# Performance work log

Measured on AMD Instinct MI355X. Metric: run time of the kernel, lower is better.

Reference implementation:

```python
import jax, jax.numpy as jnp
import numpy as np
import math

D_MODEL = 1024
N_HEAD = 16
D_HEAD = D_MODEL // N_HEAD


def setup_inputs() -> dict:
    key = jax.random.key(0)
    k0, k1, k2, k3, k4 = jax.random.split(key, 5)
    B, N = 4, 2048
    inp = jax.random.normal(k0, (B, N, D_MODEL), dtype=jnp.float32)
    # causal mask: True = keep (masked_fill on ~mask)
    mask = jnp.tril(jnp.ones((N, N), dtype=bool))
    # qkv_proj Linear(d_model, 3*d_model); output Linear(d_model, d_model)
    s_in = 1.0 / math.sqrt(D_MODEL)
    W_qkv = jax.random.uniform(k1, (D_MODEL, 3 * D_MODEL), jnp.float32, -s_in, s_in)
    b_qkv = jax.random.uniform(k2, (3 * D_MODEL,), jnp.float32, -s_in, s_in)
    W_out = jax.random.uniform(k3, (D_MODEL, D_MODEL), jnp.float32, -s_in, s_in)
    b_out = jax.random.uniform(k4, (D_MODEL,), jnp.float32, -s_in, s_in)
    return {"input": inp, "W_qkv": W_qkv, "b_qkv": b_qkv,
            "W_out": W_out, "b_out": b_out, "mask": mask}


def reference(input, W_qkv, b_qkv, W_out, b_out, mask):
    B, N, d = input.shape
    qkv = input @ W_qkv + b_qkv                       # [B,N,3d]  (dropout=eval no-op)
    q, k, v = jnp.split(qkv, 3, axis=-1)
    # [B,N,H,Dh] -> [B,H,N,Dh]
    q = q.reshape(B, N, N_HEAD, D_HEAD).transpose(0, 2, 1, 3)
    k = k.reshape(B, N, N_HEAD, D_HEAD).transpose(0, 2, 1, 3)
    v = v.reshape(B, N, N_HEAD, D_HEAD).transpose(0, 2, 1, 3)
    scale = 1.0 / math.sqrt(D_HEAD)
    scores = jnp.einsum('bhqd,bhkd->bhqk', q, k) * scale   # [B,H,N,N]
    scores = jnp.where(mask, scores, -jnp.inf)
    attn = jax.nn.softmax(scores, axis=-1)
    out = jnp.einsum('bhqk,bhkd->bhqd', attn, v)           # [B,H,N,Dh]
    out = out.transpose(0, 2, 1, 3).reshape(B, N, d)       # concat heads
    return out @ W_out + b_out
```

## Files before the change

kernel.cpp:

```cpp
#include <hip/hip_runtime.h>
#include <hip/hip_bf16.h>

typedef unsigned short u16;
typedef unsigned u32;
typedef __attribute__((ext_vector_type(4))) unsigned short u16x4;
typedef __attribute__((ext_vector_type(8))) unsigned short u16x8;
typedef __attribute__((ext_vector_type(4))) unsigned u32x4;
typedef __attribute__((ext_vector_type(8))) __bf16 bf16x8;
typedef __attribute__((ext_vector_type(4))) float f32x4;

typedef __attribute__((address_space(1))) void as1v;
typedef __attribute__((address_space(3))) void as3v;

#define MFMA16(a, b, c) __builtin_amdgcn_mfma_f32_16x16x32_bf16(a, b, c, 0, 0, 0)

__device__ __forceinline__ u16 f2bf(float f) {
    unsigned u = __builtin_bit_cast(unsigned, f);
    u += 0x7fffu + ((u >> 16) & 1u);
    return (u16)(u >> 16);
}

__device__ __forceinline__ u32 pkbf(float lo, float hi) {
    u32 r;
    asm("v_cvt_pk_bf16_f32 %0, %1, %2" : "=v"(r) : "v"(lo), "v"(hi));
    return r;
}

__device__ __forceinline__ void gload16(const void* g, void* l) {
    __builtin_amdgcn_global_load_lds((as1v*)g, (as3v*)l, 16, 0, 0);
}

__global__ void convert_f32_bf16(const float* __restrict__ in, u16* __restrict__ out, int n4) {
    int i = blockIdx.x * blockDim.x + threadIdx.x;
    if (i < n4) {
        float4 v = *(const float4*)&in[(size_t)i * 4];
        u16x4 o;
        o.x = f2bf(v.x); o.y = f2bf(v.y); o.z = f2bf(v.z); o.w = f2bf(v.w);
        *(u16x4*)&out[(size_t)i * 4] = o;
    }
}

__global__ void transpose_convert(const float* __restrict__ in, u16* __restrict__ out, int R, int C) {
    __shared__ float tl[64][65];
    const int rb = blockIdx.x, cb = blockIdx.y;
    const int tid = threadIdx.x;
    for (int it = 0; it < 4; ++it) {
        int lin = (tid + it * 256) * 4;
        int r = lin >> 6, c = lin & 63;
        float4 v = *(const float4*)&in[(size_t)(rb * 64 + r) * C + cb * 64 + c];
        tl[r][c + 0] = v.x; tl[r][c + 1] = v.y; tl[r][c + 2] = v.z; tl[r][c + 3] = v.w;
    }
    __syncthreads();
    for (int it = 0; it < 4; ++it) {
        int lin = (tid + it * 256) * 4;
        int oc = lin >> 6, orr = lin & 63;
        u16x4 o;
        o.x = f2bf(tl[orr + 0][oc]);
        o.y = f2bf(tl[orr + 1][oc]);
        o.z = f2bf(tl[orr + 2][oc]);
        o.w = f2bf(tl[orr + 3][oc]);
        *(u16x4*)&out[(size_t)(cb * 64 + oc) * R + rb * 64 + orr] = o;
    }
}

__global__ void transpose_v(const u16* __restrict__ vbuf, u16* __restrict__ vtb) {
    __shared__ u16 tl[64][65];
    const int nb = blockIdx.x, bh = blockIdx.y;
    const int tid = threadIdx.x;
    for (int it = 0; it < 2; ++it) {
        int lin = (tid + it * 256) * 8;
        int nl = lin >> 6, dh = lin & 63;
        u16x8 v = *(const u16x8*)&vbuf[((size_t)bh * 2048 + nb * 64 + nl) * 64 + dh];
#pragma unroll
        for (int j = 0; j < 8; ++j) tl[dh + j][nl] = v[j];
    }
    __syncthreads();
    for (int it = 0; it < 2; ++it) {
        int lin = (tid + it * 256) * 8;
        int dh = lin >> 6, nl = lin & 63;
        u16x8 o;
#pragma unroll
        for (int j = 0; j < 8; ++j) o[j] = tl[dh][nl + j];
        *(u16x8*)&vtb[((size_t)bh * 64 + dh) * 2048 + nb * 64 + nl] = o;
    }
}

__global__ __launch_bounds__(512, 2) void gemm256_qkv(
    const u16* __restrict__ A, const u16* __restrict__ Bt, const float* __restrict__ bias,
    u16* __restrict__ qb, u16* __restrict__ kb, u16* __restrict__ vb) {
    constexpr int K = 1024;
    constexpr int NT = 32;
    __shared__ u16 ldsu[65536];

    const int bid = blockIdx.x;
    const int swz = (bid & 7) * 48 + (bid >> 3);
    const int bm = swz / 12, bn = swz % 12;

    const int tid = threadIdx.x, wid = tid >> 6, lane = tid & 63;
    const int wr = wid >> 2, wc = wid & 3;
    const int l15 = lane & 15, lhi = lane >> 4;

    const int sslot = (lane & 7) ^ (lane >> 3);
    const int kcol = (sslot & 3) * 8;
    const int mloc = (lane >> 3) * 2 + (sslot >> 2);

    const u16* Arow[2];
    const u16* Brow[2];
#pragma unroll
    for (int li = 0; li < 2; ++li) {
        int sg = wid * 2 + li;
        int m = sg * 16 + mloc;
        Arow[li] = A + (size_t)(bm * 256 + m) * K + kcol;
        Brow[li] = Bt + (size_t)(bn * 256 + m) * K + kcol;
    }

    auto stageA = [&](int buf, int t) {
#pragma unroll
        for (int li = 0; li < 2; ++li) {
            int sg = wid * 2 + li;
            gload16(Arow[li] + t * 32, (char*)ldsu + buf * 32768 + sg * 1024);
        }
    };
    auto stageB = [&](int buf, int t) {
#pragma unroll
        for (int li = 0; li < 2; ++li) {
            int sg = wid * 2 + li;
            gload16(Brow[li] + t * 32, (char*)ldsu + buf * 32768 + 16384 + sg * 1024);
        }
    };

    const int rslot = ((l15 & 1) * 4 + lhi) ^ ((l15 >> 1) & 7);
    const int fragoff = (l15 >> 1) * 64 + rslot * 8;

    f32x4 acc[8][4];
#pragma unroll
    for (int i = 0; i < 8; ++i)
#pragma unroll
        for (int j = 0; j < 4; ++j) acc[i][j] = (f32x4){0.f, 0.f, 0.f, 0.f};

    auto doTile = [&](int cur, int tstage, bool dostage) {
        const u16* Ab = ldsu + cur * 16384 + wr * 4096 + fragoff;
        const u16* Bb = ldsu + cur * 16384 + 8192 + wc * 2048 + fragoff;
        bf16x8 af[8], b0, b1;
#pragma unroll
        for (int mf = 0; mf < 8; ++mf) af[mf] = *(const bf16x8*)(Ab + mf * 512);
        b0 = *(const bf16x8*)(Bb);
        b1 = *(const bf16x8*)(Bb + 512);
        if (dostage) stageA(tstage & 3, tstage);
        __builtin_amdgcn_s_setprio(1);
#pragma unroll
        for (int mf = 0; mf < 8; ++mf) {
            acc[mf][0] = MFMA16(af[mf], b0, acc[mf][0]);
            acc[mf][1] = MFMA16(af[mf], b1, acc[mf][1]);
        }
        __builtin_amdgcn_s_setprio(0);
        b0 = *(const bf16x8*)(Bb + 1024);
        b1 = *(const bf16x8*)(Bb + 1536);
        if (dostage) stageB(tstage & 3, tstage);
        __builtin_amdgcn_s_setprio(1);
#pragma unroll
        for (int mf = 0; mf < 8; ++mf) {
            acc[mf][2] = MFMA16(af[mf], b0, acc[mf][2]);
            acc[mf][3] = MFMA16(af[mf], b1, acc[mf][3]);
        }
        __builtin_amdgcn_s_setprio(0);
    };

    stageA(0, 0); stageB(0, 0);
    stageA(1, 1); stageB(1, 1);
    stageA(2, 2); stageB(2, 2);
    asm volatile("s_waitcnt vmcnt(8)" ::: "memory");
    __builtin_amdgcn_s_barrier();
    __builtin_amdgcn_sched_barrier(0);

    for (int t = 0; t < NT - 3; ++t) {
        doTile(t & 3, t + 3, true);
        asm volatile("s_waitcnt vmcnt(8)" ::: "memory");
        __builtin_amdgcn_s_barrier();
        __builtin_amdgcn_sched_barrier(0);
    }
    doTile((NT - 3) & 3, 0, false);
    asm volatile("s_waitcnt vmcnt(4)" ::: "memory");
    __builtin_amdgcn_s_barrier();
    __builtin_amdgcn_sched_barrier(0);
    doTile((NT - 2) & 3, 0, false);
    asm volatile("s_waitcnt vmcnt(0)" ::: "memory");
    __builtin_amdgcn_s_barrier();
    __builtin_amdgcn_sched_barrier(0);
    doTile((NT - 1) & 3, 0, false);

    const int bnbase = bn * 256 + wc * 64;
#pragma unroll
    for (int nf = 0; nf < 4; ++nf) {
        int cg = bnbase + nf * 16 + l15;
        float bv = bias[cg];
        int which = cg >> 10, rem = cg & 1023;
        u16* dst = (which == 0) ? qb : (which == 1) ? kb : vb;
        float qs = (which == 0) ? 0.18033688011112042f : 1.0f;
        size_t colterm = (size_t)(rem >> 6) * 131072 + (size_t)(rem & 63);
#pragma unroll
        for (int mf = 0; mf < 8; ++mf) {
            int rgb = bm * 256 + wr * 128 + mf * 16 + lhi * 4;
            size_t rowterm = (size_t)(rgb >> 11) * 2097152 + (size_t)(rgb & 2047) * 64;
#pragma unroll
            for (int v = 0; v < 4; ++v) {
                float val = (acc[mf][nf][v] + bv) * qs;
                dst[rowterm + (size_t)v * 64 + colterm] = f2bf(val);
            }
        }
    }
}

__global__ __launch_bounds__(256) void gemm_bt(
    const u16* __restrict__ A, const u16* __restrict__ Bt, const float* __restrict__ bias,
    int M, int N, int K, int mode,
    u16* __restrict__ qb, u16* __restrict__ kb, u16* __restrict__ vb, float* __restrict__ outf) {
    __shared__ u16 Al[128 * 32];
    __shared__ u16 Bl[128 * 32];
    const int bm = blockIdx.x, bn = blockIdx.y;
    const int tid = threadIdx.x, wid = tid >> 6, lane = tid & 63;
    const int wr = wid >> 1, wc = wid & 1;
    const int l15 = lane & 15, lhi = lane >> 4;

    f32x4 acc[4][4];
#pragma unroll
    for (int i = 0; i < 4; ++i)
#pragma unroll
        for (int j = 0; j < 4; ++j) acc[i][j] = (f32x4){0.f, 0.f, 0.f, 0.f};

    for (int k0 = 0; k0 < K; k0 += 32) {
        __syncthreads();
#pragma unroll
        for (int s = 0; s < 2; ++s) {
            int lin0 = (wid * 2 + s) * 1024;
            int off = lin0 + lane * 16;
            int row = off >> 6, colb = off & 63;
            const u16* ga = A + (size_t)(bm * 128 + row) * K + k0 + (colb >> 1);
            gload16(ga, (char*)Al + lin0);
            const u16* gb = Bt + (size_t)(bn * 128 + row) * K + k0 + (colb >> 1);
            gload16(gb, (char*)Bl + lin0);
        }
        __syncthreads();
        bf16x8 af[4], bfr[4];
#pragma unroll
        for (int mt = 0; mt < 4; ++mt)
            af[mt] = *(const bf16x8*)&Al[(wr * 64 + mt * 16 + l15) * 32 + lhi * 8];
#pragma unroll
        for (int nt = 0; nt < 4; ++nt)
            bfr[nt] = *(const bf16x8*)&Bl[(wc * 64 + nt * 16 + l15) * 32 + lhi * 8];
#pragma unroll
        for (int mt = 0; mt < 4; ++mt)
#pragma unroll
            for (int nt = 0; nt < 4; ++nt)
                acc[mt][nt] = MFMA16(af[mt], bfr[nt], acc[mt][nt]);
    }

#pragma unroll
    for (int mt = 0; mt < 4; ++mt)
#pragma unroll
        for (int nt = 0; nt < 4; ++nt)
#pragma unroll
            for (int v = 0; v < 4; ++v) {
                int rg = bm * 128 + wr * 64 + mt * 16 + lhi * 4 + v;
                int cg = bn * 128 + wc * 64 + nt * 16 + l15;
                float val = acc[mt][nt][v] + bias[cg];
                if (mode == 0) {
                    int which = cg >> 10, rem = cg & 1023;
                    int hh = rem >> 6, dh = rem & 63;
                    int bb = rg >> 11, n = rg & 2047;
                    size_t idx = (((size_t)bb * 16 + hh) * 2048 + n) * 64 + dh;
                    if (which == 0) qb[idx] = f2bf(val * 0.18033688011112042f);
                    else if (which == 1) kb[idx] = f2bf(val);
                    else vb[idx] = f2bf(val);
                } else {
                    outf[(size_t)rg * N + cg] = val;
                }
            }
}

__global__ __launch_bounds__(256, 2) void attn_kernel(
    const u16* __restrict__ qbuf, const u16* __restrict__ kbuf,
    const u16* __restrict__ vtb, u16* __restrict__ obuf) {
    __shared__ u16 Kl[2][64 * 64];
    __shared__ u16 Vl[2][64 * 64];
    const int p = blockIdx.x, bh = blockIdx.y;
    const int b = bh >> 4, h = bh & 15;
    const int tid = threadIdx.x, wid = tid >> 6, lane = tid & 63;
    const int l15 = lane & 15, lhi = lane >> 4;
    const int qA0 = p * 64 + wid * 16;
    const int qB0 = (31 - p) * 64 + wid * 16;
    const int ntA = p + 1;
    const int ntmax = 32 - p;

    bf16x8 qfA[2], qfB[2];
    {
        const u16* qa = qbuf + ((size_t)bh * 2048 + qA0 + l15) * 64 + lhi * 8;
        const u16* qbp = qbuf + ((size_t)bh * 2048 + qB0 + l15) * 64 + lhi * 8;
        qfA[0] = *(const bf16x8*)(qa);
        qfA[1] = *(const bf16x8*)(qa + 32);
        qfB[0] = *(const bf16x8*)(qbp);
        qfB[1] = *(const bf16x8*)(qbp + 32);
    }

    float mA = -1e30f, lA = 0.f, mB = -1e30f, lB = 0.f;
    f32x4 oA[4], oB[4];
#pragma unroll
    for (int d = 0; d < 4; ++d) {
        oA[d] = (f32x4){0.f, 0.f, 0.f, 0.f};
        oB[d] = (f32x4){0.f, 0.f, 0.f, 0.f};
    }

    const int srow = lane >> 3;
    const int scolb = ((lane & 7) * 16) ^ (srow << 4);

    auto stage = [&](int buf, int t) {
        const int kbase = t * 64;
#pragma unroll
        for (int s = 0; s < 2; ++s) {
            int sg = wid * 2 + s;
            int row = sg * 8 + srow;
            const u16* gk = kbuf + ((size_t)bh * 2048 + kbase + row) * 64 + (scolb >> 1);
            gload16(gk, (char*)Kl[buf] + sg * 1024);
            const u16* gv = vtb + ((size_t)bh * 64 + row) * 2048 + kbase + (scolb >> 1);
            gload16(gv, (char*)Vl[buf] + sg * 1024);
        }
    };

    auto computeTile = [&](int bufc, int t, int q0, const bf16x8* qf,
                           float& m, float& l, f32x4* oa) {
        const char* Kb = (const char*)Kl[bufc];
        const char* Vb = (const char*)Vl[bufc];
        f32x4 s[4];
        __builtin_amdgcn_s_setprio(1);
#pragma unroll
        for (int kb4 = 0; kb4 < 4; ++kb4) {
            const int r = kb4 * 16 + l15;
            const int sw = (r & 7) << 4;
            const int rowb = r * 128;
            f32x4 a = (f32x4){0.f, 0.f, 0.f, 0.f};
            a = MFMA16(*(const bf16x8*)(Kb + rowb + ((lhi * 16) ^ sw)), qf[0], a);
            a = MFMA16(*(const bf16x8*)(Kb + rowb + ((64 + lhi * 16) ^ sw)), qf[1], a);
            s[kb4] = a;
        }
        __builtin_amdgcn_s_setprio(0);
        const int qg = q0 + l15;
        if (64 * t + 63 > q0) {
#pragma unroll
            for (int kb4 = 0; kb4 < 4; ++kb4)
#pragma unroll
                for (int v = 0; v < 4; ++v) {
                    int kg = 64 * t + kb4 * 16 + lhi * 4 + v;
                    if (kg > qg) s[kb4][v] = -1e30f;
                }
        }
        float pm = fmaxf(fmaxf(fmaxf(s[0][0], s[0][1]), fmaxf(s[0][2], s[0][3])),
                         fmaxf(fmaxf(s[1][0], s[1][1]), fmaxf(s[1][2], s[1][3])));
        pm = fmaxf(pm, fmaxf(fmaxf(fmaxf(s[2][0], s[2][1]), fmaxf(s[2][2], s[2][3])),
                             fmaxf(fmaxf(s[3][0], s[3][1]), fmaxf(s[3][2], s[3][3]))));
        pm = fmaxf(pm, __shfl_xor(pm, 16, 64));
        pm = fmaxf(pm, __shfl_xor(pm, 32, 64));
        float nm = fmaxf(m, pm);
        float f = exp2f(m - nm);
        m = nm;
        float rs = 0.f;
#pragma unroll
        for (int kb4 = 0; kb4 < 4; ++kb4)
#pragma unroll
            for (int v = 0; v < 4; ++v) {
                float e = exp2f(s[kb4][v] - nm);
                s[kb4][v] = e;
                rs += e;
            }
        rs += __shfl_xor(rs, 16, 64);
        rs += __shfl_xor(rs, 32, 64);
        l = l * f + rs;
#pragma unroll
        for (int d = 0; d < 4; ++d)
#pragma unroll
            for (int v = 0; v < 4; ++v) oa[d][v] *= f;
        u32 pw0[4], pw1[4];
        pw0[0] = pkbf(s[0][0], s[0][1]); pw0[1] = pkbf(s[0][2], s[0][3]);
        pw0[2] = pkbf(s[1][0], s[1][1]); pw0[3] = pkbf(s[1][2], s[1][3]);
        pw1[0] = pkbf(s[2][0], s[2][1]); pw1[1] = pkbf(s[2][2], s[2][3]);
        pw1[2] = pkbf(s[3][0], s[3][1]); pw1[3] = pkbf(s[3][2], s[3][3]);
        __builtin_amdgcn_s_setprio(1);
#pragma unroll
        for (int ks = 0; ks < 2; ++ks) {
            bf16x8 pb = __builtin_bit_cast(bf16x8,
                ks == 0 ? (u32x4){pw0[0], pw0[1], pw0[2], pw0[3]}
                        : (u32x4){pw1[0], pw1[1], pw1[2], pw1[3]});
#pragma unroll
            for (int dhb = 0; dhb < 4; ++dhb) {
                const int r = dhb * 16 + l15;
                const int sw = (r & 7) << 4;
                u16x4 v0 = *(const u16x4*)(Vb + r * 128 + ((ks * 64 + 8 * lhi) ^ sw));
                u16x4 v1 = *(const u16x4*)(Vb + r * 128 + ((ks * 64 + 32 + 8 * lhi) ^ sw));
                u16x8 vv = {v0[0], v0[1], v0[2], v0[3], v1[0], v1[1], v1[2], v1[3]};
                oa[dhb] = MFMA16(__builtin_bit_cast(bf16x8, vv), pb, oa[dhb]);
            }
        }
        __builtin_amdgcn_s_setprio(0);
    };

    stage(0, 0);
    int cur = 0;
    for (int t = 0; t < ntmax; ++t) {
        __syncthreads();
        if (t + 1 < ntmax) stage(cur ^ 1, t + 1);
        computeTile(cur, t, qB0, qfB, mB, lB, oB);
        if (t < ntA) computeTile(cur, t, qA0, qfA, mA, lA, oA);
        cur ^= 1;
    }

    auto epi = [&](int q0, float l, const f32x4* oa) {
        const float rl = 1.f / l;
        const int q = q0 + l15;
        const size_t rowoff = ((size_t)b * 2048 + q) * 1024 + h * 64;
#pragma unroll
        for (int dhb = 0; dhb < 4; ++dhb) {
            u16x4 w;
#pragma unroll
            for (int v = 0; v < 4; ++v) w[v] = f2bf(oa[dhb][v] * rl);
            *(u16x4*)&obuf[rowoff + dhb * 16 + lhi * 4] = w;
        }
    };
    epi(qA0, lA, oA);
    epi(qB0, lB, oB);
}

extern "C" void kernel_launch(void* const* d_in, const int* in_sizes, int n_in,
                              void* d_out, int out_size, void* d_ws, size_t ws_size,
                              hipStream_t stream) {
    const float* inp   = (const float*)d_in[0];
    const float* W_qkv = (const float*)d_in[1];
    const float* b_qkv = (const float*)d_in[2];
    const float* W_out = (const float*)d_in[3];
    const float* b_out = (const float*)d_in[4];
    float* out = (float*)d_out;

    u16* xb   = (u16*)d_ws;
    u16* wqt  = xb + 8388608;
    u16* wot  = wqt + 3145728;
    u16* qbuf = wot + 1048576;
    u16* kbuf = qbuf + 8388608;
    u16* vbuf = kbuf + 8388608;
    u16* vtb  = vbuf + 8388608;
    u16* obuf = vtb + 8388608;

    convert_f32_bf16<<<8192, 256, 0, stream>>>(inp, xb, 2097152);
    transpose_convert<<<dim3(16, 48), 256, 0, stream>>>(W_qkv, wqt, 1024, 3072);
    transpose_convert<<<dim3(16, 16), 256, 0, stream>>>(W_out, wot, 1024, 1024);
    gemm256_qkv<<<384, 512, 0, stream>>>(xb, wqt, b_qkv, qbuf, kbuf, vbuf);
    transpose_v<<<dim3(32, 64), 256, 0, stream>>>(vbuf, vtb);
    attn_kernel<<<dim3(16, 64), 256, 0, stream>>>(qbuf, kbuf, vtb, obuf);
    gemm_bt<<<dim3(64, 8), 256, 0, stream>>>(obuf, wot, b_out, 8192, 1024, 1024, 1,
                                             nullptr, nullptr, nullptr, out);
}
```

Before: 206.5 us.

## Widen attention query tiles to 32 rows per wave with lazy softmax rescale

The attention kernel now assigns each wave 32 query rows (two 16-row halves) per pair tile and shares each K/V fragment read from LDS across two MFMA streams. This halves the grid to 512 blocks, remapped so consecutive blocks interleave heads. It also skips the online-softmax rescale unless the running max grows by more than 8, manually unrolls the double buffer into static indices, and strips the unused QKV mode from gemm_bt. The costs are higher register pressure, which may hurt occupancy, and a per-wave causal bound that leaves the workload less evenly balanced.

```diff
diff --git a/kernel.cpp b/kernel.cpp
--- a/kernel.cpp
+++ b/kernel.cpp
@@ -213,8 +213,7 @@
 
 __global__ __launch_bounds__(256) void gemm_bt(
     const u16* __restrict__ A, const u16* __restrict__ Bt, const float* __restrict__ bias,
-    int M, int N, int K, int mode,
-    u16* __restrict__ qb, u16* __restrict__ kb, u16* __restrict__ vb, float* __restrict__ outf) {
+    int M, int N, int K, float* __restrict__ outf) {
     __shared__ u16 Al[128 * 32];
     __shared__ u16 Bl[128 * 32];
     const int bm = blockIdx.x, bn = blockIdx.y;
@@ -263,18 +262,7 @@
             for (int v = 0; v < 4; ++v) {
                 int rg = bm * 128 + wr * 64 + mt * 16 + lhi * 4 + v;
                 int cg = bn * 128 + wc * 64 + nt * 16 + l15;
-                float val = acc[mt][nt][v] + bias[cg];
-                if (mode == 0) {
-                    int which = cg >> 10, rem = cg & 1023;
-                    int hh = rem >> 6, dh = rem & 63;
-                    int bb = rg >> 11, n = rg & 2047;
-                    size_t idx = (((size_t)bb * 16 + hh) * 2048 + n) * 64 + dh;
-                    if (which == 0) qb[idx] = f2bf(val * 0.18033688011112042f);
-                    else if (which == 1) kb[idx] = f2bf(val);
-                    else vb[idx] = f2bf(val);
-                } else {
-                    outf[(size_t)rg * N + cg] = val;
-                }
+                outf[(size_t)rg * N + cg] = acc[mt][nt][v] + bias[cg];
             }
 }
 
@@ -283,31 +271,34 @@
     const u16* __restrict__ vtb, u16* __restrict__ obuf) {
     __shared__ u16 Kl[2][64 * 64];
     __shared__ u16 Vl[2][64 * 64];
-    const int p = blockIdx.x, bh = blockIdx.y;
+    const int bid = blockIdx.x;
+    const int c = (bid >> 3) & 7;
+    const int bh = ((bid & 7) << 3) + (bid >> 6);
     const int b = bh >> 4, h = bh & 15;
     const int tid = threadIdx.x, wid = tid >> 6, lane = tid & 63;
     const int l15 = lane & 15, lhi = lane >> 4;
-    const int qA0 = p * 64 + wid * 16;
-    const int qB0 = (31 - p) * 64 + wid * 16;
-    const int ntA = p + 1;
-    const int ntmax = 32 - p;
-
-    bf16x8 qfA[2], qfB[2];
-    {
-        const u16* qa = qbuf + ((size_t)bh * 2048 + qA0 + l15) * 64 + lhi * 8;
-        const u16* qbp = qbuf + ((size_t)bh * 2048 + qB0 + l15) * 64 + lhi * 8;
-        qfA[0] = *(const bf16x8*)(qa);
-        qfA[1] = *(const bf16x8*)(qa + 32);
-        qfB[0] = *(const bf16x8*)(qbp);
-        qfB[1] = *(const bf16x8*)(qbp + 32);
-    }
-
-    float mA = -1e30f, lA = 0.f, mB = -1e30f, lB = 0.f;
-    f32x4 oA[4], oB[4];
+    const int qA0 = c * 128 + wid * 32;
+    const int qB0 = (15 - c) * 128 + wid * 32;
+    const int ntA = 2 * c + (wid >> 1) + 1;
+    const int ntB = 31 - 2 * c + (wid >> 1);
+    const int ntmax = 32 - 2 * c;
+
+    auto loadQ = [&](int qbase, bf16x8* dst) {
+        const u16* qp = qbuf + ((size_t)bh * 2048 + qbase + l15) * 64 + lhi * 8;
+        dst[0] = *(const bf16x8*)(qp);
+        dst[1] = *(const bf16x8*)(qp + 32);
+    };
+    bf16x8 qfA0[2], qfA1[2], qfB0[2], qfB1[2];
+    loadQ(qA0, qfA0); loadQ(qA0 + 16, qfA1);
+    loadQ(qB0, qfB0); loadQ(qB0 + 16, qfB1);
+
+    float mA0 = -1e30f, lA0 = 0.f, mA1 = -1e30f, lA1 = 0.f;
+    float mB0 = -1e30f, lB0 = 0.f, mB1 = -1e30f, lB1 = 0.f;
+    f32x4 oA0[4], oA1[4], oB0[4], oB1[4];
 #pragma unroll
     for (int d = 0; d < 4; ++d) {
-        oA[d] = (f32x4){0.f, 0.f, 0.f, 0.f};
-        oB[d] = (f32x4){0.f, 0.f, 0.f, 0.f};
+        oA0[d] = (f32x4){0.f, 0.f, 0.f, 0.f}; oA1[d] = (f32x4){0.f, 0.f, 0.f, 0.f};
+        oB0[d] = (f32x4){0.f, 0.f, 0.f, 0.f}; oB1[d] = (f32x4){0.f, 0.f, 0.f, 0.f};
     }
 
     const int srow = lane >> 3;
@@ -326,25 +317,9 @@
         }
     };
 
-    auto computeTile = [&](int bufc, int t, int q0, const bf16x8* qf,
-                           float& m, float& l, f32x4* oa) {
-        const char* Kb = (const char*)Kl[bufc];
-        const char* Vb = (const char*)Vl[bufc];
-        f32x4 s[4];
-        __builtin_amdgcn_s_setprio(1);
-#pragma unroll
-        for (int kb4 = 0; kb4 < 4; ++kb4) {
-            const int r = kb4 * 16 + l15;
-            const int sw = (r & 7) << 4;
-            const int rowb = r * 128;
-            f32x4 a = (f32x4){0.f, 0.f, 0.f, 0.f};
-            a = MFMA16(*(const bf16x8*)(Kb + rowb + ((lhi * 16) ^ sw)), qf[0], a);
-            a = MFMA16(*(const bf16x8*)(Kb + rowb + ((64 + lhi * 16) ^ sw)), qf[1], a);
-            s[kb4] = a;
-        }
-        __builtin_amdgcn_s_setprio(0);
-        const int qg = q0 + l15;
-        if (64 * t + 63 > q0) {
+    auto smax = [&](f32x4* s, int qg0, int t, float& m, float& l, f32x4* oa, u32* pw) {
+        const int qg = qg0 + l15;
+        if (64 * t + 63 > qg0) {
 #pragma unroll
             for (int kb4 = 0; kb4 < 4; ++kb4)
 #pragma unroll
@@ -359,36 +334,67 @@
                              fmaxf(fmaxf(s[3][0], s[3][1]), fmaxf(s[3][2], s[3][3]))));
         pm = fmaxf(pm, __shfl_xor(pm, 16, 64));
         pm = fmaxf(pm, __shfl_xor(pm, 32, 64));
-        float nm = fmaxf(m, pm);
-        float f = exp2f(m - nm);
-        m = nm;
+        if (!__all(pm <= m + 8.f)) {
+            float nm = fmaxf(m, pm);
+            float f = exp2f(m - nm);
+            m = nm;
+            l *= f;
+#pragma unroll
+            for (int d = 0; d < 4; ++d)
+#pragma unroll
+                for (int v = 0; v < 4; ++v) oa[d][v] *= f;
+        }
         float rs = 0.f;
 #pragma unroll
         for (int kb4 = 0; kb4 < 4; ++kb4)
 #pragma unroll
             for (int v = 0; v < 4; ++v) {
-                float e = exp2f(s[kb4][v] - nm);
+                float e = exp2f(s[kb4][v] - m);
                 s[kb4][v] = e;
                 rs += e;
             }
         rs += __shfl_xor(rs, 16, 64);
         rs += __shfl_xor(rs, 32, 64);
-        l = l * f + rs;
-#pragma unroll
-        for (int d = 0; d < 4; ++d)
-#pragma unroll
-            for (int v = 0; v < 4; ++v) oa[d][v] *= f;
-        u32 pw0[4], pw1[4];
-        pw0[0] = pkbf(s[0][0], s[0][1]); pw0[1] = pkbf(s[0][2], s[0][3]);
-        pw0[2] = pkbf(s[1][0], s[1][1]); pw0[3] = pkbf(s[1][2], s[1][3]);
-        pw1[0] = pkbf(s[2][0], s[2][1]); pw1[1] = pkbf(s[2][2], s[2][3]);
-        pw1[2] = pkbf(s[3][0], s[3][1]); pw1[3] = pkbf(s[3][2], s[3][3]);
+        l += rs;
+        pw[0] = pkbf(s[0][0], s[0][1]); pw[1] = pkbf(s[0][2], s[0][3]);
+        pw[2] = pkbf(s[1][0], s[1][1]); pw[3] = pkbf(s[1][2], s[1][3]);
+        pw[4] = pkbf(s[2][0], s[2][1]); pw[5] = pkbf(s[2][2], s[2][3]);
+        pw[6] = pkbf(s[3][0], s[3][1]); pw[7] = pkbf(s[3][2], s[3][3]);
+    };
+
+    auto computeChunk = [&](const char* Kb, const char* Vb, int t, int q0,
+                            const bf16x8* qf0, const bf16x8* qf1,
+                            float& m0, float& l0, f32x4* oa0,
+                            float& m1, float& l1, f32x4* oa1) {
+        f32x4 s0[4], s1[4];
         __builtin_amdgcn_s_setprio(1);
 #pragma unroll
+        for (int kb4 = 0; kb4 < 4; ++kb4) {
+            const int r = kb4 * 16 + l15;
+            const int sw = (r & 7) << 4;
+            const int rowb = r * 128;
+            bf16x8 kf0 = *(const bf16x8*)(Kb + rowb + ((lhi * 16) ^ sw));
+            bf16x8 kf1 = *(const bf16x8*)(Kb + rowb + ((64 + lhi * 16) ^ sw));
+            f32x4 a0 = (f32x4){0.f, 0.f, 0.f, 0.f};
+            a0 = MFMA16(kf0, qf0[0], a0);
+            a0 = MFMA16(kf1, qf0[1], a0);
+            s0[kb4] = a0;
+            f32x4 a1 = (f32x4){0.f, 0.f, 0.f, 0.f};
+            a1 = MFMA16(kf0, qf1[0], a1);
+            a1 = MFMA16(kf1, qf1[1], a1);
+            s1[kb4] = a1;
+        }
+        __builtin_amdgcn_s_setprio(0);
+        u32 pw0[8], pw1[8];
+        smax(s0, q0, t, m0, l0, oa0, pw0);
+        smax(s1, q0 + 16, t, m1, l1, oa1, pw1);
+        __builtin_amdgcn_s_setprio(1);
+#pragma unroll
         for (int ks = 0; ks < 2; ++ks) {
-            bf16x8 pb = __builtin_bit_cast(bf16x8,
-                ks == 0 ? (u32x4){pw0[0], pw0[1], pw0[2], pw0[3]}
-                        : (u32x4){pw1[0], pw1[1], pw1[2], pw1[3]});
+            bf16x8 pb0 = __builtin_bit_cast(bf16x8,
+                (u32x4){pw0[ks * 4 + 0], pw0[ks * 4 + 1], pw0[ks * 4 + 2], pw0[ks * 4 + 3]});
+            bf16x8 pb1 = __builtin_bit_cast(bf16x8,
+                (u32x4){pw1[ks * 4 + 0], pw1[ks * 4 + 1], pw1[ks * 4 + 2], pw1[ks * 4 + 3]});
 #pragma unroll
             for (int dhb = 0; dhb < 4; ++dhb) {
                 const int r = dhb * 16 + l15;
@@ -396,20 +402,30 @@
                 u16x4 v0 = *(const u16x4*)(Vb + r * 128 + ((ks * 64 + 8 * lhi) ^ sw));
                 u16x4 v1 = *(const u16x4*)(Vb + r * 128 + ((ks * 64 + 32 + 8 * lhi) ^ sw));
                 u16x8 vv = {v0[0], v0[1], v0[2], v0[3], v1[0], v1[1], v1[2], v1[3]};
-                oa[dhb] = MFMA16(__builtin_bit_cast(bf16x8, vv), pb, oa[dhb]);
+                bf16x8 vf = __builtin_bit_cast(bf16x8, vv);
+                oa0[dhb] = MFMA16(vf, pb0, oa0[dhb]);
+                oa1[dhb] = MFMA16(vf, pb1, oa1[dhb]);
             }
         }
         __builtin_amdgcn_s_setprio(0);
     };
 
+    auto step = [&](const char* Kb, const char* Vb, int t) {
+        if (t < ntB) computeChunk(Kb, Vb, t, qB0, qfB0, qfB1, mB0, lB0, oB0, mB1, lB1, oB1);
+        if (t < ntA) computeChunk(Kb, Vb, t, qA0, qfA0, qfA1, mA0, lA0, oA0, mA1, lA1, oA1);
+    };
+
     stage(0, 0);
-    int cur = 0;
-    for (int t = 0; t < ntmax; ++t) {
+    int t = 0;
+    for (;;) {
         __syncthreads();
-        if (t + 1 < ntmax) stage(cur ^ 1, t + 1);
-        computeTile(cur, t, qB0, qfB, mB, lB, oB);
-        if (t < ntA) computeTile(cur, t, qA0, qfA, mA, lA, oA);
-        cur ^= 1;
+        if (t + 1 < ntmax) stage(1, t + 1);
+        step((const char*)Kl[0], (const char*)Vl[0], t);
+        if (++t == ntmax) break;
+        __syncthreads();
+        if (t + 1 < ntmax) stage(0, t + 1);
+        step((const char*)Kl[1], (const char*)Vl[1], t);
+        if (++t == ntmax) break;
     }
 
     auto epi = [&](int q0, float l, const f32x4* oa) {
@@ -424,8 +440,10 @@
             *(u16x4*)&obuf[rowoff + dhb * 16 + lhi * 4] = w;
         }
     };
-    epi(qA0, lA, oA);
-    epi(qB0, lB, oB);
+    epi(qA0, lA0, oA0);
+    epi(qA0 + 16, lA1, oA1);
+    epi(qB0, lB0, oB0);
+    epi(qB0 + 16, lB1, oB1);
 }
 
 extern "C" void kernel_launch(void* const* d_in, const int* in_sizes, int n_in,
@@ -452,7 +470,6 @@
     transpose_convert<<<dim3(16, 16), 256, 0, stream>>>(W_out, wot, 1024, 1024);
     gemm256_qkv<<<384, 512, 0, stream>>>(xb, wqt, b_qkv, qbuf, kbuf, vbuf);
     transpose_v<<<dim3(32, 64), 256, 0, stream>>>(vbuf, vtb);
-    attn_kernel<<<dim3(16, 64), 256, 0, stream>>>(qbuf, kbuf, vtb, obuf);
-    gemm_bt<<<dim3(64, 8), 256, 0, stream>>>(obuf, wot, b_out, 8192, 1024, 1024, 1,
-                                             nullptr, nullptr, nullptr, out);
-}
+    attn_kernel<<<512, 256, 0, stream>>>(qbuf, kbuf, vtb, obuf);
+    gemm_bt<<<dim3(64, 8), 256, 0, stream>>>(obuf, wot, b_out, 8192, 1024, 1024, out);
+}
```

Measured after the change: 203.1 us. No clear change (-1.6%).
